# Performance work log

Measured on AMD Instinct MI355X. Metric: run time of the kernel, lower is better.

Reference implementation:

```python
import math
import jax, jax.numpy as jnp
import numpy as np

HEADS = 8

def relative_shift(score):
    # score: [B, H, S, 2S-1] -> [B, H, S, S] via Music Transformer skew trick
    B, H, S, R = score.shape
    score = jnp.pad(score, ((0, 0), (0, 0), (0, 0), (1, 0)))          # [B,H,S,2S]
    score = score.reshape(B, H, -1)[:, :, S:].reshape(B, H, S, -1)    # [B,H,S,2S-1]
    return score[..., :S]


def setup_inputs() -> dict:
    B, S, D = 4, 1024, 512
    dh = D // HEADS
    rng = jax.random.key(0)
    ks = jax.random.split(rng, 14)
    w = 0.02  # init scale
    return {
        "query":   jax.random.normal(ks[0], (B, S, D), jnp.float32),
        "key":     jax.random.normal(ks[1], (B, S, D), jnp.float32),
        "value":   jax.random.normal(ks[2], (B, S, D), jnp.float32),
        "pos_emb": jax.random.normal(ks[3], (2 * S - 1, dh), jnp.float32),
        "Wq": jax.random.normal(ks[4], (D, D), jnp.float32) * w,
        "bq": jnp.zeros((D,), jnp.float32),
        "Wk": jax.random.normal(ks[5], (D, D), jnp.float32) * w,
        "bk": jnp.zeros((D,), jnp.float32),
        "Wv": jax.random.normal(ks[6], (D, D), jnp.float32) * w,
        "bv": jnp.zeros((D,), jnp.float32),
        "Wo": jax.random.normal(ks[7], (D, D), jnp.float32) * w,
        "bo": jnp.zeros((D,), jnp.float32),
        "Wp": jax.random.normal(ks[8], (dh, dh), jnp.float32) * w,
        "bp": jnp.zeros((dh,), jnp.float32),
    }


def reference(query, key, value, pos_emb, Wq, bq, Wk, bk, Wv, bv, Wo, bo, Wp, bp):
    B, S, D = query.shape
    H = HEADS
    dh = D // H
    q = (query @ Wq.T + bq).reshape(B, S, H, dh).transpose(0, 2, 1, 3)  # [B,H,S,dh]
    k = (key   @ Wk.T + bk).reshape(B, S, H, dh).transpose(0, 2, 1, 3)  # [B,H,S,dh]
    v = (value @ Wv.T + bv).reshape(B, S, H, dh).transpose(0, 2, 1, 3)  # [B,H,S,dh]
    rel = pos_emb @ Wp.T + bp                                           # [2S-1, dh]

    pos_score = jnp.einsum('bhsd,rd->bhsr', q, rel)                     # [B,H,S,2S-1]
    pos_score = relative_shift(pos_score)                               # [B,H,S,S]
    content_score = jnp.einsum('bhsd,bhtd->bhst', q, k)                 # [B,H,S,S]
    score = (content_score + pos_score) / math.sqrt(D)                  # scale by sqrt(d_model)
    attn = jax.nn.softmax(score, axis=-1)
    out = jnp.einsum('bhst,bhtd->bshd', attn, v).reshape(B, S, D)
    return (out @ Wo.T + bo, attn, content_score, pos_score)
```

## Files before the change

kernel.cpp:

```cpp
#include <hip/hip_runtime.h>

typedef __attribute__((ext_vector_type(8))) short short8;
typedef __attribute__((ext_vector_type(4))) float f32x4;
typedef unsigned short u16;
typedef unsigned int u32;

#define MFMA16(a, b, c) __builtin_amdgcn_mfma_f32_16x16x32_bf16((a), (b), (c), 0, 0, 0)
#define SCALE 0.044194173824159216f

__device__ __forceinline__ u16 f2bf(float f) {
    u32 u = __float_as_uint(f);
    u = (u + 0x7fffu + ((u >> 16) & 1u)) >> 16;
    return (u16)u;
}

__global__ __launch_bounds__(256) void cvt_kernel(const float* __restrict__ src,
                                                  u16* __restrict__ dst, int n4) {
    int i = blockIdx.x * 256 + threadIdx.x;
    if (i >= n4) return;
    float4 v = ((const float4*)src)[i];
    unsigned long long p = (unsigned long long)f2bf(v.x)
                         | ((unsigned long long)f2bf(v.y) << 16)
                         | ((unsigned long long)f2bf(v.z) << 32)
                         | ((unsigned long long)f2bf(v.w) << 48);
    ((unsigned long long*)dst)[i] = p;
}

__global__ __launch_bounds__(256) void rel_kernel(const float* __restrict__ pos_emb,
                                                  const float* __restrict__ Wp,
                                                  const float* __restrict__ bp,
                                                  u16* __restrict__ rel) {
    int idx = blockIdx.x * 256 + threadIdx.x;
    if (idx >= 2047 * 64) return;
    int r = idx >> 6, c = idx & 63;
    const float* pe = pos_emb + r * 64;
    const float* w  = Wp + c * 64;
    float acc = bp[c];
#pragma unroll
    for (int k = 0; k < 64; k++) acc += pe[k] * w[k];
    rel[r * 64 + c] = f2bf(acc);
}

template <int MODE>
__global__ __launch_bounds__(256) void gemm_kernel(const u16* __restrict__ A,
                                                   const u16* __restrict__ B,
                                                   const float* __restrict__ bias,
                                                   void* __restrict__ Cout,
                                                   int M, int N, int K) {
    int tid = threadIdx.x;
    int w = tid >> 6, lane = tid & 63;
    int wi = w >> 1, wj = w & 1;
    int qd = lane >> 4, ln = lane & 15;
    int m_base = blockIdx.x * 64 + wi * 32;
    int n_base = blockIdx.y * 64 + wj * 32;
    f32x4 acc[2][2] = {};
    const u16* a0p = A + (long)(m_base + ln) * K + qd * 8;
    const u16* a1p = a0p + 16 * K;
    const u16* b0p = B + (long)(n_base + ln) * K + qd * 8;
    const u16* b1p = b0p + 16 * K;
    for (int kc = 0; kc < K; kc += 32) {
        short8 a0 = *(const short8*)(a0p + kc);
        short8 a1 = *(const short8*)(a1p + kc);
        short8 b0 = *(const short8*)(b0p + kc);
        short8 b1 = *(const short8*)(b1p + kc);
        acc[0][0] = MFMA16(a0, b0, acc[0][0]);
        acc[0][1] = MFMA16(a0, b1, acc[0][1]);
        acc[1][0] = MFMA16(a1, b0, acc[1][0]);
        acc[1][1] = MFMA16(a1, b1, acc[1][1]);
    }
#pragma unroll
    for (int i = 0; i < 2; i++)
#pragma unroll
        for (int j = 0; j < 2; j++)
#pragma unroll
            for (int r = 0; r < 4; r++) {
                int m = m_base + i * 16 + qd * 4 + r;
                int n = n_base + j * 16 + ln;
                float v = acc[i][j][r];
                if (MODE == 0) {
                    v += bias[n];
                    int b = m >> 10, s = m & 1023, h = n >> 6, d = n & 63;
                    ((u16*)Cout)[(((long)(b * 8 + h) << 10) + s) * 64 + d] = f2bf(v);
                } else if (MODE == 1) {
                    v += bias[m];
                    int b = n >> 10, t = n & 1023, h = m >> 6, d = m & 63;
                    ((u16*)Cout)[(((long)(b * 8 + h) * 64 + d) << 10) + t] = f2bf(v);
                } else {
                    v += bias[n];
                    ((float*)Cout)[(long)m * N + n] = v;
                }
            }
}

__global__ __launch_bounds__(256) void score_kernel(const u16* __restrict__ qws,
                                                    const u16* __restrict__ kws,
                                                    const u16* __restrict__ vtws,
                                                    const u16* __restrict__ relws,
                                                    float* __restrict__ out_attn,
                                                    float* __restrict__ out_cont,
                                                    float* __restrict__ out_pos,
                                                    u16* __restrict__ ctx) {
    __shared__ float sc[16][1024];
    int st = blockIdx.x, h = blockIdx.y, b = blockIdx.z;
    int s0 = st * 16;
    int tid = threadIdx.x;
    int w = tid >> 6, lane = tid & 63, qd = lane >> 4, ln = lane & 15;
    int bh = b * 8 + h;

    const u16* qbase  = qws + ((long)bh << 10) * 64;
    const u16* kbase  = kws + ((long)bh << 10) * 64;
    const u16* vtbase = vtws + ((long)bh << 6) * 1024;
    float* attn_base = out_attn + ((long)bh << 20) + (long)s0 * 1024;
    float* cont_base = out_cont + ((long)bh << 20) + (long)s0 * 1024;
    float* pos_base  = out_pos  + ((long)bh << 20) + (long)s0 * 1024;

    short8 qa0 = *(const short8*)(qbase + (s0 + ln) * 64 + qd * 8);
    short8 qa1 = *(const short8*)(qbase + (s0 + ln) * 64 + 32 + qd * 8);

    for (int tt = 0; tt < 16; tt++) {
        int t0 = w * 256 + tt * 16;
        short8 kb0 = *(const short8*)(kbase + (t0 + ln) * 64 + qd * 8);
        short8 kb1 = *(const short8*)(kbase + (t0 + ln) * 64 + 32 + qd * 8);
        f32x4 acc = {};
        acc = MFMA16(qa0, kb0, acc);
        acc = MFMA16(qa1, kb1, acc);
#pragma unroll
        for (int r = 0; r < 4; r++) {
            int sl = qd * 4 + r;
            int t = t0 + ln;
            cont_base[sl * 1024 + t] = acc[r];
            sc[sl][t] = acc[r] * SCALE;
        }
    }
    __syncthreads();

    int rbase = 1008 - s0;
    for (int rt = w; rt < 65; rt += 4) {
        int r0 = rbase + rt * 16;
        short8 rb0 = *(const short8*)(relws + (r0 + ln) * 64 + qd * 8);
        short8 rb1 = *(const short8*)(relws + (r0 + ln) * 64 + 32 + qd * 8);
        f32x4 acc = {};
        acc = MFMA16(qa0, rb0, acc);
        acc = MFMA16(qa1, rb1, acc);
#pragma unroll
        for (int r = 0; r < 4; r++) {
            int sl = qd * 4 + r;
            int t = rt * 16 + ln + sl - 15;
            if (t >= 0 && t < 1024) {
                pos_base[sl * 1024 + t] = acc[r];
                sc[sl][t] += acc[r] * SCALE;
            }
        }
    }
    __syncthreads();

    {
        int row = tid >> 4;
        int g = tid & 15;
        float ev[64];
        float mx = -1e30f;
#pragma unroll
        for (int i = 0; i < 64; i++) {
            float v = sc[row][g + 16 * i];
            ev[i] = v;
            mx = fmaxf(mx, v);
        }
        for (int off = 1; off < 16; off <<= 1) mx = fmaxf(mx, __shfl_xor(mx, off, 64));
        float sum = 0.f;
#pragma unroll
        for (int i = 0; i < 64; i++) {
            float e = __expf(ev[i] - mx);
            ev[i] = e;
            sum += e;
        }
        for (int off = 1; off < 16; off <<= 1) sum += __shfl_xor(sum, off, 64);
        float inv = 1.0f / sum;
#pragma unroll
        for (int i = 0; i < 64; i++) {
            float a = ev[i] * inv;
            sc[row][g + 16 * i] = a;
            attn_base[row * 1024 + g + 16 * i] = a;
        }
    }
    __syncthreads();

    {
        const u16* vrow = vtbase + (w * 16 + ln) * 1024 + qd * 8;
        f32x4 oacc = {};
        for (int kt = 0; kt < 32; kt++) {
            const f32x4* ap = (const f32x4*)(&sc[ln][kt * 32 + qd * 8]);
            f32x4 x = ap[0], y = ap[1];
            short8 a;
            a[0] = (short)f2bf(x[0]); a[1] = (short)f2bf(x[1]);
            a[2] = (short)f2bf(x[2]); a[3] = (short)f2bf(x[3]);
            a[4] = (short)f2bf(y[0]); a[5] = (short)f2bf(y[1]);
            a[6] = (short)f2bf(y[2]); a[7] = (short)f2bf(y[3]);
            short8 bf = *(const short8*)(vrow + kt * 32);
            oacc = MFMA16(a, bf, oacc);
        }
#pragma unroll
        for (int r = 0; r < 4; r++) {
            int sl = qd * 4 + r;
            int d = w * 16 + ln;
            ctx[((long)(b * 1024 + s0 + sl)) * 512 + h * 64 + d] = f2bf(oacc[r]);
        }
    }
}

extern "C" void kernel_launch(void* const* d_in, const int* in_sizes, int n_in,
                              void* d_out, int out_size, void* d_ws, size_t ws_size,
                              hipStream_t stream) {
    (void)in_sizes; (void)n_in; (void)out_size; (void)ws_size;
    const float* query   = (const float*)d_in[0];
    const float* key     = (const float*)d_in[1];
    const float* value   = (const float*)d_in[2];
    const float* pos_emb = (const float*)d_in[3];
    const float* Wq = (const float*)d_in[4];
    const float* bq = (const float*)d_in[5];
    const float* Wk = (const float*)d_in[6];
    const float* bk = (const float*)d_in[7];
    const float* Wv = (const float*)d_in[8];
    const float* bv = (const float*)d_in[9];
    const float* Wo = (const float*)d_in[10];
    const float* bo = (const float*)d_in[11];
    const float* Wp = (const float*)d_in[12];
    const float* bp = (const float*)d_in[13];

    u16* qin  = (u16*)d_ws;
    u16* kin  = qin + 4096 * 512;
    u16* vin  = kin + 4096 * 512;
    u16* wqb  = vin + 4096 * 512;
    u16* wkb  = wqb + 512 * 512;
    u16* wvb  = wkb + 512 * 512;
    u16* wob  = wvb + 512 * 512;
    u16* relb = wob + 512 * 512;
    u16* qws  = relb + 2048 * 64;
    u16* kws  = qws + 4 * 8 * 1024 * 64;
    u16* vtws = kws + 4 * 8 * 1024 * 64;
    u16* ctx  = qin;

    float* out  = (float*)d_out;
    float* attn = out + 2097152;
    float* cont = attn + 33554432;
    float* pos  = cont + 33554432;

    cvt_kernel<<<2048, 256, 0, stream>>>(query, qin, 524288);
    cvt_kernel<<<2048, 256, 0, stream>>>(key, kin, 524288);
    cvt_kernel<<<2048, 256, 0, stream>>>(value, vin, 524288);
    cvt_kernel<<<256, 256, 0, stream>>>(Wq, wqb, 65536);
    cvt_kernel<<<256, 256, 0, stream>>>(Wk, wkb, 65536);
    cvt_kernel<<<256, 256, 0, stream>>>(Wv, wvb, 65536);
    cvt_kernel<<<256, 256, 0, stream>>>(Wo, wob, 65536);
    rel_kernel<<<512, 256, 0, stream>>>(pos_emb, Wp, bp, relb);

    gemm_kernel<0><<<dim3(64, 8), 256, 0, stream>>>(qin, wqb, bq, qws, 4096, 512, 512);
    gemm_kernel<0><<<dim3(64, 8), 256, 0, stream>>>(kin, wkb, bk, kws, 4096, 512, 512);
    gemm_kernel<1><<<dim3(8, 64), 256, 0, stream>>>(wvb, vin, bv, vtws, 512, 4096, 512);

    score_kernel<<<dim3(64, 8, 4), 256, 0, stream>>>(qws, kws, vtws, relb, attn, cont, pos, ctx);

    gemm_kernel<2><<<dim3(64, 8), 256, 0, stream>>>(ctx, wob, bo, out, 4096, 512, 512);
}
```

Measured before the change: 240.7 us.

## Swizzle score LDS, vectorize softmax IO, pack bf16 probabilities in LDS

Applies an XOR swizzle to the shared score tile so that column-strided writes from the MFMA results avoid bank conflicts. The softmax pass now reads and writes float2 pairs, writing attn to global memory as 8-byte stores. The normalized probabilities are converted once to bf16 with v_cvt_pk_bf16_f32 and stored in a swizzled bf16 view of the same shared buffer, which removes the per-iteration fp32-to-bf16 conversion in the PV MFMA loop. An extra barrier is needed because the bf16 view aliases the fp32 scores.

```diff
diff --git a/kernel.cpp b/kernel.cpp
--- a/kernel.cpp
+++ b/kernel.cpp
@@ -2,11 +2,15 @@
 
 typedef __attribute__((ext_vector_type(8))) short short8;
 typedef __attribute__((ext_vector_type(4))) float f32x4;
+typedef __attribute__((ext_vector_type(2))) float f32x2;
 typedef unsigned short u16;
 typedef unsigned int u32;
 
 #define MFMA16(a, b, c) __builtin_amdgcn_mfma_f32_16x16x32_bf16((a), (b), (c), 0, 0, 0)
 #define SCALE 0.044194173824159216f
+
+#define SCX(r, c) ((c) ^ (((r) & 7) << 2))
+#define PAX(r, c) ((c) ^ (((r) & 7) << 3))
 
 __device__ __forceinline__ u16 f2bf(float f) {
     u32 u = __float_as_uint(f);
@@ -100,7 +104,8 @@
                                                     float* __restrict__ out_cont,
                                                     float* __restrict__ out_pos,
                                                     u16* __restrict__ ctx) {
-    __shared__ float sc[16][1024];
+    __shared__ __align__(16) float sc[16][1024];
+    u16* pa = (u16*)sc;
     int st = blockIdx.x, h = blockIdx.y, b = blockIdx.z;
     int s0 = st * 16;
     int tid = threadIdx.x;
@@ -129,7 +134,7 @@
             int sl = qd * 4 + r;
             int t = t0 + ln;
             cont_base[sl * 1024 + t] = acc[r];
-            sc[sl][t] = acc[r] * SCALE;
+            sc[sl][SCX(sl, t)] = acc[r] * SCALE;
         }
     }
     __syncthreads();
@@ -148,7 +153,7 @@
             int t = rt * 16 + ln + sl - 15;
             if (t >= 0 && t < 1024) {
                 pos_base[sl * 1024 + t] = acc[r];
-                sc[sl][t] += acc[r] * SCALE;
+                sc[sl][SCX(sl, t)] += acc[r] * SCALE;
             }
         }
     }
@@ -160,10 +165,12 @@
         float ev[64];
         float mx = -1e30f;
 #pragma unroll
-        for (int i = 0; i < 64; i++) {
-            float v = sc[row][g + 16 * i];
-            ev[i] = v;
-            mx = fmaxf(mx, v);
+        for (int i = 0; i < 32; i++) {
+            int c = 2 * g + 32 * i;
+            f32x2 v = *(const f32x2*)&sc[row][SCX(row, c)];
+            ev[2 * i] = v[0];
+            ev[2 * i + 1] = v[1];
+            mx = fmaxf(mx, fmaxf(v[0], v[1]));
         }
         for (int off = 1; off < 16; off <<= 1) mx = fmaxf(mx, __shfl_xor(mx, off, 64));
         float sum = 0.f;
@@ -175,11 +182,17 @@
         }
         for (int off = 1; off < 16; off <<= 1) sum += __shfl_xor(sum, off, 64);
         float inv = 1.0f / sum;
-#pragma unroll
-        for (int i = 0; i < 64; i++) {
-            float a = ev[i] * inv;
-            sc[row][g + 16 * i] = a;
-            attn_base[row * 1024 + g + 16 * i] = a;
+        __syncthreads();
+#pragma unroll
+        for (int i = 0; i < 32; i++) {
+            int c = 2 * g + 32 * i;
+            float a0 = ev[2 * i] * inv;
+            float a1 = ev[2 * i + 1] * inv;
+            f32x2 av = {a0, a1};
+            *(f32x2*)&attn_base[row * 1024 + c] = av;
+            u32 pk;
+            asm("v_cvt_pk_bf16_f32 %0, %1, %2" : "=v"(pk) : "v"(a0), "v"(a1));
+            *(u32*)&pa[row * 1024 + PAX(row, c)] = pk;
         }
     }
     __syncthreads();
@@ -188,13 +201,8 @@
         const u16* vrow = vtbase + (w * 16 + ln) * 1024 + qd * 8;
         f32x4 oacc = {};
         for (int kt = 0; kt < 32; kt++) {
-            const f32x4* ap = (const f32x4*)(&sc[ln][kt * 32 + qd * 8]);
-            f32x4 x = ap[0], y = ap[1];
-            short8 a;
-            a[0] = (short)f2bf(x[0]); a[1] = (short)f2bf(x[1]);
-            a[2] = (short)f2bf(x[2]); a[3] = (short)f2bf(x[3]);
-            a[4] = (short)f2bf(y[0]); a[5] = (short)f2bf(y[1]);
-            a[6] = (short)f2bf(y[2]); a[7] = (short)f2bf(y[3]);
+            int c = kt * 32 + qd * 8;
+            short8 a = *(const short8*)&pa[ln * 1024 + PAX(ln, c)];
             short8 bf = *(const short8*)(vrow + kt * 32);
             oacc = MFMA16(a, bf, oacc);
         }
```

Result: faster. 225.2 us (-6.4%).
